# Performance work log

Measured on AMD Instinct MI355X. Metric: run time of the kernel, lower is better.

Reference implementation:

```python
import jax, jax.numpy as jnp
import numpy as np

N_NODES = 50000
N_EDGES = 800000
HID = 128
EDGE_IN = 2 * HID + 4 + 20  # 2*hidden + edge_feat_dim + num_r_gaussian = 280


def setup_inputs() -> dict:
    key = jax.random.key(0)
    ks = jax.random.split(key, 16)
    s = lambda fan_in: 1.0 / np.sqrt(fan_in)
    inp = {
        "h": jax.random.normal(ks[0], (N_NODES, HID), dtype=jnp.float32),
        "edge_index": jax.random.randint(ks[1], (2, N_EDGES), 0, N_NODES, dtype=jnp.int64) if jax.config.jax_enable_x64 else jax.random.randint(ks[1], (2, N_EDGES), 0, N_NODES, dtype=jnp.int32),
        "edge_attr": jax.random.normal(ks[2], (N_EDGES, 24), dtype=jnp.float32),
        # edge_mlp: Linear(280->128) relu Linear(128->128) relu (act_last=True)
        "We1": jax.random.uniform(ks[3], (EDGE_IN, HID), jnp.float32, -s(EDGE_IN), s(EDGE_IN)),
        "be1": jnp.zeros((HID,), jnp.float32),
        "We2": jax.random.uniform(ks[4], (HID, HID), jnp.float32, -s(HID), s(HID)),
        "be2": jnp.zeros((HID,), jnp.float32),
        # edge_inf: Linear(128->1) + sigmoid
        "Wg": jax.random.uniform(ks[5], (HID, 1), jnp.float32, -s(HID), s(HID)),
        "bg": jnp.zeros((1,), jnp.float32),
        # node_mlp: Linear(256->128) relu Linear(128->128)
        "Wn1": jax.random.uniform(ks[6], (2 * HID, HID), jnp.float32, -s(2 * HID), s(2 * HID)),
        "bn1": jnp.zeros((HID,), jnp.float32),
        "Wn2": jax.random.uniform(ks[7], (HID, HID), jnp.float32, -s(HID), s(HID)),
        "bn2": jnp.zeros((HID,), jnp.float32),
    }
    return inp


def reference(h, edge_index, edge_attr, We1, be1, We2, be2, Wg, bg, Wn1, bn1, Wn2, bn2):
    dst, src = edge_index[0], edge_index[1]
    hi, hj = h[dst], h[src]                       # [E, HID] each
    x = jnp.concatenate([edge_attr, hi, hj], -1)  # [E, 280]
    mij = jax.nn.relu(jax.nn.relu(x @ We1 + be1) @ We2 + be2)  # [E, HID]
    eij = jax.nn.sigmoid(mij @ Wg + bg)           # [E, 1]
    mi = jax.ops.segment_sum(mij * eij, dst, num_segments=h.shape[0])  # [N, HID]
    y = jnp.concatenate([mi, h], -1)              # [N, 2*HID]
    out = jax.nn.relu(y @ Wn1 + bn1) @ Wn2 + bn2  # [N, HID]
    return out
```

## Files before the change

### kernel.cpp

```cpp
#include <hip/hip_runtime.h>

#define N_NODES 50000
#define N_EDGES 800000
#define HID 128

typedef _Float16 f16;
typedef _Float16 half8 __attribute__((ext_vector_type(8)));
typedef _Float16 half4 __attribute__((ext_vector_type(4)));
typedef _Float16 half2v __attribute__((ext_vector_type(2)));
typedef float f32x4 __attribute__((ext_vector_type(4)));
typedef float f32x2 __attribute__((ext_vector_type(2)));

#define OFF_MI     0UL
#define OFF_H16C   25600000UL
#define OFF_WC     38400000UL
#define OFF_CNT    38604800UL
#define OFF_OFFS   38805504UL
#define OFF_CUR    39006208UL
#define OFF_PERM   39206912UL
#define CSR_TOTAL  42406912UL

#define OFF_FMI  0UL
#define OFF_FH16 25600000UL
#define OFF_FW   38400000UL

#define WB1 0
#define WB2 36864
#define WN1 53248
#define WN2 86016

#define TS 136
#define YS 264
#define SS 132
#define AS 40

#define EB 32

__global__ __launch_bounds__(256) void pack_weights(
    const float* __restrict__ We1, const float* __restrict__ We2,
    const float* __restrict__ Wn1, const float* __restrict__ Wn2,
    f16* __restrict__ W, int* __restrict__ cnt) {
  int i = blockIdx.x * 256 + threadIdx.x;
  if (cnt && i < 50176) cnt[i] = 0;
  if (i < 36864) {
    int j = i & 7, n = (i >> 3) & 127, qk = i >> 10;
    int k = qk * 8 + j;
    float v = 0.f;
    if (k < 256) v = We1[(24 + k) * 128 + n];
    else if (k < 280) v = We1[(k - 256) * 128 + n];
    W[WB1 + i] = (f16)v;
  } else if (i < 53248) {
    int l = i - 36864;
    int j = l & 7, n = (l >> 3) & 127, qk = l >> 10;
    W[WB2 + l] = (f16)We2[(qk * 8 + j) * 128 + n];
  } else if (i < 86016) {
    int l = i - 53248;
    int j = l & 7, n = (l >> 3) & 127, qk = l >> 10;
    W[WN1 + l] = (f16)Wn1[(qk * 8 + j) * 128 + n];
  } else if (i < 102400) {
    int l = i - 86016;
    int j = l & 7, n = (l >> 3) & 127, qk = l >> 10;
    W[WN2 + l] = (f16)Wn2[(qk * 8 + j) * 128 + n];
  }
}

__global__ __launch_bounds__(256) void scan_kernel(const int* __restrict__ cnt,
                                                   int* __restrict__ offs, int* __restrict__ cur) {
  __shared__ int sb[256];
  int t = threadIdx.x;
  int base = t * 196;
  int s = 0;
  for (int k = 0; k < 196; ++k) s += cnt[base + k];
  sb[t] = s;
  __syncthreads();
  for (int off = 1; off < 256; off <<= 1) {
    int v = (t >= off) ? sb[t - off] : 0;
    __syncthreads();
    sb[t] += v;
    __syncthreads();
  }
  int run = sb[t] - s;
  for (int k = 0; k < 196; ++k) {
    int c = cnt[base + k];
    offs[base + k] = run;
    cur[base + k] = run;
    run += c;
  }
}

__global__ __launch_bounds__(256) void fill_perm(
    const int* __restrict__ eidx, int* __restrict__ cur, int* __restrict__ perm) {
  int i = blockIdx.x * 256 + threadIdx.x;
  int p = atomicAdd(&cur[eidx[i]], 1);
  perm[p] = i;
}

__global__ __launch_bounds__(256, 4) void precompute_kernel(
    const float* __restrict__ h, const int* __restrict__ eidx,
    const f16* __restrict__ Wp, f16* __restrict__ P,
    f16* __restrict__ h16, int* __restrict__ cnt) {
  __shared__ f16 Y[64 * 136];
  int t = threadIdx.x;
  int n0 = blockIdx.x * 64;
  {
    int rb = t >> 4, ch = t & 15;
    for (int p = 0; p < 4; ++p) {
      int r = p * 16 + rb;
      int g = n0 + r; if (g >= N_NODES) g = N_NODES - 1;
      const float4* s4 = (const float4*)(h + (size_t)g * HID + ch * 8);
      float4 a = s4[0], b = s4[1];
      half8 v = {(f16)a.x, (f16)a.y, (f16)a.z, (f16)a.w,
                 (f16)b.x, (f16)b.y, (f16)b.z, (f16)b.w};
      *(half8*)&Y[r * 136 + ch * 8] = v;
      *(half8*)(h16 + (size_t)g * HID + ch * 8) = v;
    }
  }
  if (cnt) {
    for (int i = blockIdx.x * 256 + t; i < N_EDGES; i += gridDim.x * 256)
      atomicAdd(&cnt[eidx[i]], 1);
  }
  __syncthreads();
  int w = t >> 6, lane = t & 63, q = lane >> 4, c = lane & 15;
  int colBase = w * 32;
  const f16* B = Wp + WB1 + ((size_t)(q * 128 + colBase + c)) * 8;
  f32x4 aD[4][2], aS[4][2];
  #pragma unroll
  for (int mt = 0; mt < 4; ++mt) {
    aD[mt][0] = (f32x4){0, 0, 0, 0}; aD[mt][1] = (f32x4){0, 0, 0, 0};
    aS[mt][0] = (f32x4){0, 0, 0, 0}; aS[mt][1] = (f32x4){0, 0, 0, 0};
  }
  #pragma unroll
  for (int ks = 0; ks < 4; ++ks) {
    half8 bD0 = *(const half8*)(B + ks * 4096);
    half8 bD1 = *(const half8*)(B + ks * 4096 + 128);
    half8 bS0 = *(const half8*)(B + (ks + 4) * 4096);
    half8 bS1 = *(const half8*)(B + (ks + 4) * 4096 + 128);
    #pragma unroll
    for (int mt = 0; mt < 4; ++mt) {
      half8 a = *(const half8*)&Y[(mt * 16 + c) * 136 + ks * 32 + q * 8];
      aD[mt][0] = __builtin_amdgcn_mfma_f32_16x16x32_f16(a, bD0, aD[mt][0], 0, 0, 0);
      aD[mt][1] = __builtin_amdgcn_mfma_f32_16x16x32_f16(a, bD1, aD[mt][1], 0, 0, 0);
      aS[mt][0] = __builtin_amdgcn_mfma_f32_16x16x32_f16(a, bS0, aS[mt][0], 0, 0, 0);
      aS[mt][1] = __builtin_amdgcn_mfma_f32_16x16x32_f16(a, bS1, aS[mt][1], 0, 0, 0);
    }
  }
  #pragma unroll
  for (int mt = 0; mt < 4; ++mt)
    #pragma unroll
    for (int r = 0; r < 4; ++r) {
      int g = n0 + mt * 16 + q * 4 + r;
      if (g < N_NODES) {
        f16* o = P + (size_t)g * 256 + colBase + c;
        o[0]        = (f16)aD[mt][0][r];
        o[16]       = (f16)aD[mt][1][r];
        o[128]      = (f16)aS[mt][0][r];
        o[128 + 16] = (f16)aS[mt][1][r];
      }
    }
}

__global__ __launch_bounds__(256, 8) void edge_kernel(
    const f16* __restrict__ P, const int* __restrict__ eidx,
    const float* __restrict__ eattr,
    const f16* __restrict__ Wp, const float* __restrict__ be1,
    const float* __restrict__ be2,
    const float* __restrict__ Wg, const float* __restrict__ bg,
    float* __restrict__ mi, const int* __restrict__ perm) {
  __shared__ float S[EB * SS];
  __shared__ f16 A[EB * AS];
  __shared__ float part[EB * 4];
  __shared__ float eijL[EB];
  __shared__ int dstL[EB];
  int t = threadIdx.x;
  int e0 = blockIdx.x * EB;

  if (t < EB) {
    int e = perm ? perm[e0 + t] : (e0 + t);
    dstL[t] = eidx[e];
  }
  {
    int rb = t >> 4, ch = t & 15;
    for (int p = 0; p < 2; ++p) {
      int r = p * 16 + rb;
      int e = perm ? perm[e0 + r] : (e0 + r);
      int d = eidx[e];
      int s = eidx[N_EDGES + e];
      half8 pd = *(const half8*)(P + (size_t)d * 256 + ch * 8);
      half8 ps = *(const half8*)(P + (size_t)s * 256 + 128 + ch * 8);
      f32x4 lo = {(float)pd[0] + (float)ps[0], (float)pd[1] + (float)ps[1],
                  (float)pd[2] + (float)ps[2], (float)pd[3] + (float)ps[3]};
      f32x4 hi = {(float)pd[4] + (float)ps[4], (float)pd[5] + (float)ps[5],
                  (float)pd[6] + (float)ps[6], (float)pd[7] + (float)ps[7]};
      *(f32x4*)&S[r * SS + ch * 8]     = lo;
      *(f32x4*)&S[r * SS + ch * 8 + 4] = hi;
    }
  }
  if (t < 192) {
    int el = t / 6, kk = t % 6;
    int e = perm ? perm[e0 + el] : (e0 + el);
    float4 f = *(const float4*)(eattr + (size_t)e * 24 + kk * 4);
    half4 hv = {(f16)f.x, (f16)f.y, (f16)f.z, (f16)f.w};
    *(half4*)&A[el * AS + kk * 4] = hv;
  }
  if (t < EB) { uint4 z = {0, 0, 0, 0}; *(uint4*)&A[t * AS + 24] = z; }
  __syncthreads();

  int w = t >> 6, lane = t & 63, q = lane >> 4, c = lane & 15;
  int colBase = w * 32;

  f32x4 acc[2][2];
  {
    float b0 = be1[colBase + c], b1 = be1[colBase + 16 + c];
    #pragma unroll
    for (int mt = 0; mt < 2; ++mt) {
      acc[mt][0] = (f32x4){b0, b0, b0, b0};
      acc[mt][1] = (f32x4){b1, b1, b1, b1};
    }
  }
  {
    const f16* bA = Wp + WB1 + 32768 + ((size_t)(q * 128 + colBase + c)) * 8;
    half8 b0f = *(const half8*)(bA);
    half8 b1f = *(const half8*)(bA + 128);
    #pragma unroll
    for (int mt = 0; mt < 2; ++mt) {
      half8 a = *(const half8*)&A[(mt * 16 + c) * AS + q * 8];
      acc[mt][0] = __builtin_amdgcn_mfma_f32_16x16x32_f16(a, b0f, acc[mt][0], 0, 0, 0);
      acc[mt][1] = __builtin_amdgcn_mfma_f32_16x16x32_f16(a, b1f, acc[mt][1], 0, 0, 0);
    }
  }
  #pragma unroll
  for (int mt = 0; mt < 2; ++mt)
    #pragma unroll
    for (int r = 0; r < 4; ++r) {
      const float* sr = &S[(mt * 16 + q * 4 + r) * SS + colBase + c];
      acc[mt][0][r] += sr[0];
      acc[mt][1][r] += sr[16];
    }

  const f16* bp2base = Wp + WB2 + ((size_t)(q * 128 + colBase + c)) * 8;
  half8 d0 = *(const half8*)(bp2base);
  half8 d1 = *(const half8*)(bp2base + 128);

  __syncthreads();
  f16* T = (f16*)S;
  #pragma unroll
  for (int mt = 0; mt < 2; ++mt)
    #pragma unroll
    for (int nt = 0; nt < 2; ++nt)
      #pragma unroll
      for (int r = 0; r < 4; ++r) {
        float v = acc[mt][nt][r];
        T[(mt * 16 + q * 4 + r) * TS + colBase + nt * 16 + c] = (f16)(v > 0.f ? v : 0.f);
      }
  __syncthreads();

  f32x4 m2[2][2];
  {
    float b0 = be2[colBase + c], b1 = be2[colBase + 16 + c];
    #pragma unroll
    for (int mt = 0; mt < 2; ++mt) {
      m2[mt][0] = (f32x4){b0, b0, b0, b0};
      m2[mt][1] = (f32x4){b1, b1, b1, b1};
    }
  }
  #pragma unroll
  for (int kk = 0; kk < 4; ++kk) {
    half8 n0, n1;
    if (kk < 3) {
      n0 = *(const half8*)(bp2base + (kk + 1) * 4096);
      n1 = *(const half8*)(bp2base + (kk + 1) * 4096 + 128);
    }
    #pragma unroll
    for (int mt = 0; mt < 2; ++mt) {
      half8 a = *(const half8*)&T[(mt * 16 + c) * TS + kk * 32 + q * 8];
      m2[mt][0] = __builtin_amdgcn_mfma_f32_16x16x32_f16(a, d0, m2[mt][0], 0, 0, 0);
      m2[mt][1] = __builtin_amdgcn_mfma_f32_16x16x32_f16(a, d1, m2[mt][1], 0, 0, 0);
    }
    d0 = n0; d1 = n1;
  }

  float wg0 = Wg[colBase + c], wg1 = Wg[colBase + 16 + c];
  float pd[2][4];
  #pragma unroll
  for (int mt = 0; mt < 2; ++mt)
    #pragma unroll
    for (int r = 0; r < 4; ++r) {
      float v0 = m2[mt][0][r]; v0 = v0 > 0.f ? v0 : 0.f; m2[mt][0][r] = v0;
      float v1 = m2[mt][1][r]; v1 = v1 > 0.f ? v1 : 0.f; m2[mt][1][r] = v1;
      pd[mt][r] = v0 * wg0 + v1 * wg1;
    }
  #pragma unroll
  for (int off = 1; off < 16; off <<= 1)
    #pragma unroll
    for (int mt = 0; mt < 2; ++mt)
      #pragma unroll
      for (int r = 0; r < 4; ++r)
        pd[mt][r] += __shfl_xor(pd[mt][r], off, 64);
  if (c == 0)
    #pragma unroll
    for (int mt = 0; mt < 2; ++mt)
      #pragma unroll
      for (int r = 0; r < 4; ++r)
        part[(mt * 16 + q * 4 + r) * 4 + w] = pd[mt][r];
  __syncthreads();
  if (t < EB) {
    float s = part[t * 4] + part[t * 4 + 1] + part[t * 4 + 2] + part[t * 4 + 3] + bg[0];
    eijL[t] = 1.f / (1.f + __expf(-s));
  }
  __syncthreads();

  if (perm) {
    #pragma unroll
    for (int mt = 0; mt < 2; ++mt)
      #pragma unroll
      for (int r = 0; r < 4; ++r) {
        int el = mt * 16 + q * 4 + r;
        float ev = eijL[el];
        T[el * TS + colBase + c]      = (f16)(m2[mt][0][r] * ev);
        T[el * TS + colBase + 16 + c] = (f16)(m2[mt][1][r] * ev);
      }
    __syncthreads();
    int col = t & 127, half = t >> 7;
    int r0 = half * 16;
    float acc2 = 0.f;
    int dprev = dstL[r0];
    #pragma unroll
    for (int r2 = 0; r2 < 16; ++r2) {
      int rr = r0 + r2;
      acc2 += (float)T[rr * TS + col];
      int dnext = (r2 == 15) ? -1 : dstL[rr + 1];
      if (dnext != dprev) {
        atomicAdd(&mi[(size_t)dprev * HID + col], acc2);
        acc2 = 0.f;
        dprev = dnext;
      }
    }
  } else {
    #pragma unroll
    for (int mt = 0; mt < 2; ++mt)
      #pragma unroll
      for (int r = 0; r < 4; ++r) {
        int el = mt * 16 + q * 4 + r;
        float ev = eijL[el];
        float* base = mi + (size_t)dstL[el] * HID + colBase + c;
        atomicAdd(base,      m2[mt][0][r] * ev);
        atomicAdd(base + 16, m2[mt][1][r] * ev);
      }
  }
}

__global__ __launch_bounds__(256, 4) void node_kernel(
    const float* __restrict__ mi, const f16* __restrict__ h16,
    const f16* __restrict__ Wp, const float* __restrict__ bn1,
    const float* __restrict__ bn2, float* __restrict__ out) {
  __shared__ f16 Y[64 * YS];
  int t = threadIdx.x;
  int n0 = blockIdx.x * 64;
  {
    int rb = t >> 4, ch = t & 15;
    for (int p = 0; p < 4; ++p) {
      int r = p * 16 + rb;
      int g = n0 + r; if (g >= N_NODES) g = N_NODES - 1;
      const float4* s = (const float4*)(mi + (size_t)g * HID + ch * 8);
      float4 a = s[0], b = s[1];
      half8 v = {(f16)a.x, (f16)a.y, (f16)a.z, (f16)a.w,
                 (f16)b.x, (f16)b.y, (f16)b.z, (f16)b.w};
      *(half8*)&Y[r * YS + ch * 8] = v;
      *(uint4*)&Y[r * YS + 128 + ch * 8] = *(const uint4*)(h16 + (size_t)g * HID + ch * 8);
    }
  }
  __syncthreads();
  int w = t >> 6, lane = t & 63, q = lane >> 4, c = lane & 15;
  int colBase = w * 32;
  const f16* BN1 = Wp + WN1;
  const f16* BN2 = Wp + WN2;
  f32x4 acc[4][2];
  {
    float b0 = bn1[colBase + c], b1 = bn1[colBase + 16 + c];
    #pragma unroll
    for (int mt = 0; mt < 4; ++mt) {
      acc[mt][0] = (f32x4){b0, b0, b0, b0};
      acc[mt][1] = (f32x4){b1, b1, b1, b1};
    }
  }
  const f16* bn1base = BN1 + ((size_t)(q * 128 + colBase + c)) * 8;
  half8 bf0 = *(const half8*)(bn1base);
  half8 bf1 = *(const half8*)(bn1base + 128);
  #pragma unroll
  for (int ks = 0; ks < 8; ++ks) {
    half8 nb0, nb1;
    if (ks < 7) {
      nb0 = *(const half8*)(bn1base + (ks + 1) * 4096);
      nb1 = *(const half8*)(bn1base + (ks + 1) * 4096 + 128);
    }
    #pragma unroll
    for (int mt = 0; mt < 4; ++mt) {
      half8 a = *(const half8*)&Y[(mt * 16 + c) * YS + ks * 32 + q * 8];
      acc[mt][0] = __builtin_amdgcn_mfma_f32_16x16x32_f16(a, bf0, acc[mt][0], 0, 0, 0);
      acc[mt][1] = __builtin_amdgcn_mfma_f32_16x16x32_f16(a, bf1, acc[mt][1], 0, 0, 0);
    }
    bf0 = nb0; bf1 = nb1;
  }
  const f16* bn2base = BN2 + ((size_t)(q * 128 + colBase + c)) * 8;
  half8 d0 = *(const half8*)(bn2base);
  half8 d1 = *(const half8*)(bn2base + 128);
  __syncthreads();
  f16* T = Y;
  #pragma unroll
  for (int mt = 0; mt < 4; ++mt)
    #pragma unroll
    for (int nt = 0; nt < 2; ++nt)
      #pragma unroll
      for (int r = 0; r < 4; ++r) {
        float v = acc[mt][nt][r];
        T[(mt * 16 + q * 4 + r) * TS + colBase + nt * 16 + c] = (f16)(v > 0.f ? v : 0.f);
      }
  __syncthreads();
  f32x4 m2[4][2];
  {
    float b0 = bn2[colBase + c], b1 = bn2[colBase + 16 + c];
    #pragma unroll
    for (int mt = 0; mt < 4; ++mt) {
      m2[mt][0] = (f32x4){b0, b0, b0, b0};
      m2[mt][1] = (f32x4){b1, b1, b1, b1};
    }
  }
  #pragma unroll
  for (int kk = 0; kk < 4; ++kk) {
    half8 n0, n1;
    if (kk < 3) {
      n0 = *(const half8*)(bn2base + (kk + 1) * 4096);
      n1 = *(const half8*)(bn2base + (kk + 1) * 4096 + 128);
    }
    #pragma unroll
    for (int mt = 0; mt < 4; ++mt) {
      half8 a = *(const half8*)&T[(mt * 16 + c) * TS + kk * 32 + q * 8];
      m2[mt][0] = __builtin_amdgcn_mfma_f32_16x16x32_f16(a, d0, m2[mt][0], 0, 0, 0);
      m2[mt][1] = __builtin_amdgcn_mfma_f32_16x16x32_f16(a, d1, m2[mt][1], 0, 0, 0);
    }
    d0 = n0; d1 = n1;
  }
  #pragma unroll
  for (int mt = 0; mt < 4; ++mt)
    #pragma unroll
    for (int r = 0; r < 4; ++r) {
      int g = n0 + mt * 16 + q * 4 + r;
      if (g < N_NODES) {
        float* o = out + (size_t)g * HID + colBase + c;
        o[0]  = m2[mt][0][r];
        o[16] = m2[mt][1][r];
      }
    }
}

extern "C" void kernel_launch(void* const* d_in, const int* in_sizes, int n_in,
                              void* d_out, int out_size, void* d_ws, size_t ws_size,
                              hipStream_t stream) {
  const float* h    = (const float*)d_in[0];
  const int*   eidx = (const int*)d_in[1];
  const float* eattr= (const float*)d_in[2];
  const float* We1  = (const float*)d_in[3];
  const float* be1  = (const float*)d_in[4];
  const float* We2  = (const float*)d_in[5];
  const float* be2  = (const float*)d_in[6];
  const float* Wg   = (const float*)d_in[7];
  const float* bg   = (const float*)d_in[8];
  const float* Wn1  = (const float*)d_in[9];
  const float* bn1  = (const float*)d_in[10];
  const float* Wn2  = (const float*)d_in[11];
  const float* bn2  = (const float*)d_in[12];
  float* out = (float*)d_out;
  char* ws = (char*)d_ws;

  if (ws_size >= CSR_TOTAL) {
    float* mi  = (float*)(ws + OFF_MI);
    f16* h16   = (f16*)(ws + OFF_H16C);
    f16* Wp    = (f16*)(ws + OFF_WC);
    int* cnt   = (int*)(ws + OFF_CNT);
    int* offs  = (int*)(ws + OFF_OFFS);
    int* cur   = (int*)(ws + OFF_CUR);
    int* perm  = (int*)(ws + OFF_PERM);
    f16* P     = (f16*)out;

    hipMemsetAsync(mi, 0, (size_t)N_NODES * HID * sizeof(float), stream);
    pack_weights<<<400, 256, 0, stream>>>(We1, We2, Wn1, Wn2, Wp, cnt);
    precompute_kernel<<<(N_NODES + 63) / 64, 256, 0, stream>>>(h, eidx, Wp, P, h16, cnt);
    scan_kernel<<<1, 256, 0, stream>>>(cnt, offs, cur);
    fill_perm<<<3125, 256, 0, stream>>>(eidx, cur, perm);
    edge_kernel<<<N_EDGES / EB, 256, 0, stream>>>(P, eidx, eattr, Wp, be1, be2,
                                                  Wg, bg, mi, perm);
    node_kernel<<<(N_NODES + 63) / 64, 256, 0, stream>>>(mi, h16, Wp, bn1, bn2, out);
  } else {
    float* mi  = (float*)(ws + OFF_FMI);
    f16*   h16 = (f16*)(ws + OFF_FH16);
    f16*   Wp  = (f16*)(ws + OFF_FW);
    f16*   P   = (f16*)out;

    hipMemsetAsync(mi, 0, (size_t)N_NODES * HID * sizeof(float), stream);
    pack_weights<<<400, 256, 0, stream>>>(We1, We2, Wn1, Wn2, Wp, nullptr);
    precompute_kernel<<<(N_NODES + 63) / 64, 256, 0, stream>>>(h, eidx, Wp, P, h16, nullptr);
    edge_kernel<<<N_EDGES / EB, 256, 0, stream>>>(P, eidx, eattr, Wp, be1, be2,
                                                  Wg, bg, mi, nullptr);
    node_kernel<<<(N_NODES + 63) / 64, 256, 0, stream>>>(mi, h16, Wp, bn1, bn2, out);
  }
}
```

Baseline: 424.1 us.

## Parallelize CSR prefix scan across blocks and store gathered edge sums in fp16

Replaces the single-block serial prefix scan over node counts with a three-pass multi-block scan (per-block wave-shuffle scan, block-total scan, add-back), and drops the unused offs array. In the edge kernel, the gathered dst+src projections are summed in fp16 and staged in a half-precision shared buffer instead of fp32, halving LDS footprint and store traffic. The scan change removes a long serial single-block launch at the cost of two extra kernel launches; the fp16 sum adds a small rounding error before the fp32 accumulation.

```diff
diff --git a/kernel.cpp b/kernel.cpp
--- a/kernel.cpp
+++ b/kernel.cpp
@@ -15,10 +15,10 @@
 #define OFF_H16C   25600000UL
 #define OFF_WC     38400000UL
 #define OFF_CNT    38604800UL
-#define OFF_OFFS   38805504UL
-#define OFF_CUR    39006208UL
-#define OFF_PERM   39206912UL
-#define CSR_TOTAL  42406912UL
+#define OFF_CUR    38805504UL
+#define OFF_PERM   39006208UL
+#define OFF_BT     42206208UL
+#define CSR_TOTAL  42206464UL
 
 #define OFF_FMI  0UL
 #define OFF_FH16 25600000UL
@@ -31,7 +31,6 @@
 
 #define TS 136
 #define YS 264
-#define SS 132
 #define AS 40
 
 #define EB 32
@@ -64,28 +63,50 @@
   }
 }
 
-__global__ __launch_bounds__(256) void scan_kernel(const int* __restrict__ cnt,
-                                                   int* __restrict__ offs, int* __restrict__ cur) {
-  __shared__ int sb[256];
-  int t = threadIdx.x;
-  int base = t * 196;
-  int s = 0;
-  for (int k = 0; k < 196; ++k) s += cnt[base + k];
-  sb[t] = s;
-  __syncthreads();
-  for (int off = 1; off < 256; off <<= 1) {
-    int v = (t >= off) ? sb[t - off] : 0;
-    __syncthreads();
-    sb[t] += v;
-    __syncthreads();
-  }
-  int run = sb[t] - s;
-  for (int k = 0; k < 196; ++k) {
-    int c = cnt[base + k];
-    offs[base + k] = run;
-    cur[base + k] = run;
-    run += c;
-  }
+__global__ __launch_bounds__(256) void scanA(const int* __restrict__ cnt,
+                                             int* __restrict__ cur, int* __restrict__ bt) {
+  __shared__ int wsum[4];
+  int t = threadIdx.x, b = blockIdx.x;
+  int base = b * 1024 + t * 4;
+  int4 v = *(const int4*)(cnt + base);
+  int s = v.x + v.y + v.z + v.w;
+  int lane = t & 63, w = t >> 6;
+  int inc = s;
+  #pragma unroll
+  for (int off = 1; off < 64; off <<= 1) {
+    int u = __shfl_up(inc, off, 64);
+    if (lane >= off) inc += u;
+  }
+  if (lane == 63) wsum[w] = inc;
+  __syncthreads();
+  int wbase = 0;
+  for (int i = 0; i < w; ++i) wbase += wsum[i];
+  int excl = wbase + inc - s;
+  int4 o;
+  o.x = excl; o.y = excl + v.x; o.z = o.y + v.y; o.w = o.z + v.z;
+  *(int4*)(cur + base) = o;
+  if (t == 255) bt[b] = wbase + inc;
+}
+
+__global__ __launch_bounds__(64) void scanB(int* __restrict__ bt) {
+  int l = threadIdx.x;
+  int v = (l < 49) ? bt[l] : 0;
+  int inc = v;
+  #pragma unroll
+  for (int off = 1; off < 64; off <<= 1) {
+    int u = __shfl_up(inc, off, 64);
+    if (l >= off) inc += u;
+  }
+  if (l < 49) bt[l] = inc - v;
+}
+
+__global__ __launch_bounds__(256) void scanC(int* __restrict__ cur, const int* __restrict__ bt) {
+  int t = threadIdx.x, b = blockIdx.x;
+  int base = b * 1024 + t * 4;
+  int add = bt[b];
+  int4 o = *(int4*)(cur + base);
+  o.x += add; o.y += add; o.z += add; o.w += add;
+  *(int4*)(cur + base) = o;
 }
 
 __global__ __launch_bounds__(256) void fill_perm(
@@ -166,7 +187,7 @@
     const float* __restrict__ be2,
     const float* __restrict__ Wg, const float* __restrict__ bg,
     float* __restrict__ mi, const int* __restrict__ perm) {
-  __shared__ float S[EB * SS];
+  __shared__ f16 S16[EB * TS];
   __shared__ f16 A[EB * AS];
   __shared__ float part[EB * 4];
   __shared__ float eijL[EB];
@@ -187,12 +208,7 @@
       int s = eidx[N_EDGES + e];
       half8 pd = *(const half8*)(P + (size_t)d * 256 + ch * 8);
       half8 ps = *(const half8*)(P + (size_t)s * 256 + 128 + ch * 8);
-      f32x4 lo = {(float)pd[0] + (float)ps[0], (float)pd[1] + (float)ps[1],
-                  (float)pd[2] + (float)ps[2], (float)pd[3] + (float)ps[3]};
-      f32x4 hi = {(float)pd[4] + (float)ps[4], (float)pd[5] + (float)ps[5],
-                  (float)pd[6] + (float)ps[6], (float)pd[7] + (float)ps[7]};
-      *(f32x4*)&S[r * SS + ch * 8]     = lo;
-      *(f32x4*)&S[r * SS + ch * 8 + 4] = hi;
+      *(half8*)&S16[r * TS + ch * 8] = pd + ps;
     }
   }
   if (t < 192) {
@@ -232,9 +248,9 @@
   for (int mt = 0; mt < 2; ++mt)
     #pragma unroll
     for (int r = 0; r < 4; ++r) {
-      const float* sr = &S[(mt * 16 + q * 4 + r) * SS + colBase + c];
-      acc[mt][0][r] += sr[0];
-      acc[mt][1][r] += sr[16];
+      const f16* sr = &S16[(mt * 16 + q * 4 + r) * TS + colBase + c];
+      acc[mt][0][r] += (float)sr[0];
+      acc[mt][1][r] += (float)sr[16];
     }
 
   const f16* bp2base = Wp + WB2 + ((size_t)(q * 128 + colBase + c)) * 8;
@@ -242,7 +258,7 @@
   half8 d1 = *(const half8*)(bp2base + 128);
 
   __syncthreads();
-  f16* T = (f16*)S;
+  f16* T = S16;
   #pragma unroll
   for (int mt = 0; mt < 2; ++mt)
     #pragma unroll
@@ -477,15 +493,17 @@
     f16* h16   = (f16*)(ws + OFF_H16C);
     f16* Wp    = (f16*)(ws + OFF_WC);
     int* cnt   = (int*)(ws + OFF_CNT);
-    int* offs  = (int*)(ws + OFF_OFFS);
     int* cur   = (int*)(ws + OFF_CUR);
     int* perm  = (int*)(ws + OFF_PERM);
+    int* bt    = (int*)(ws + OFF_BT);
     f16* P     = (f16*)out;
 
     hipMemsetAsync(mi, 0, (size_t)N_NODES * HID * sizeof(float), stream);
     pack_weights<<<400, 256, 0, stream>>>(We1, We2, Wn1, Wn2, Wp, cnt);
     precompute_kernel<<<(N_NODES + 63) / 64, 256, 0, stream>>>(h, eidx, Wp, P, h16, cnt);
-    scan_kernel<<<1, 256, 0, stream>>>(cnt, offs, cur);
+    scanA<<<49, 256, 0, stream>>>(cnt, cur, bt);
+    scanB<<<1, 64, 0, stream>>>(bt);
+    scanC<<<49, 256, 0, stream>>>(cur, bt);
     fill_perm<<<3125, 256, 0, stream>>>(eidx, cur, perm);
     edge_kernel<<<N_EDGES / EB, 256, 0, stream>>>(P, eidx, eattr, Wp, be1, be2,
                                                   Wg, bg, mi, perm);
```

Result: faster. 404.6 us (-4.6%).
